# Performance work log

Hardware: AMD Instinct MI355X
Metric: run time of the kernel (lower is better)

## Reference

```python
import jax, jax.numpy as jnp
import numpy as np
import math

B, T, D_IN, D_OUT = 4, 2048, 2048, 2048

def _inv_sigmoid(v):
    return math.log(v / (1 - v + 1e-08))

def setup_inputs() -> dict:
    key = jax.random.key(0)
    ks = jax.random.split(key, 6)
    x = jax.random.normal(ks[0], (B, T, D_IN), dtype=jnp.float32)
    W_p = jax.random.normal(ks[1], (D_OUT, D_IN), dtype=jnp.float32) * 0.02
    W_i = jax.random.normal(ks[2], (D_OUT, D_IN), dtype=jnp.float32) * 0.002
    W_d = jax.random.normal(ks[3], (D_OUT, D_IN), dtype=jnp.float32) * 0.002
    alpha_logit = jnp.full((D_IN,), _inv_sigmoid(0.9), dtype=jnp.float32)
    beta_logit = jnp.full((D_IN,), _inv_sigmoid(0.5), dtype=jnp.float32)
    W_gate_w = jax.random.normal(ks[4], (3, 3 * D_IN), dtype=jnp.float32) * 0.01
    W_gate_b = jnp.array([1.0, 0.0, 0.0], dtype=jnp.float32)
    bias = jnp.zeros((D_OUT,), dtype=jnp.float32)
    return {"x": x, "W_p": W_p, "W_i": W_i, "W_d": W_d,
            "alpha_logit": alpha_logit, "beta_logit": beta_logit,
            "W_gate_w": W_gate_w, "W_gate_b": W_gate_b, "bias": bias}

def _pid_features(x, alpha, beta):
    # x: (B,T,D). Single scan computing EMA integral and smoothed derivative.
    x_t = jnp.swapaxes(x, 0, 1)  # (T,B,D)
    x_prev = jnp.concatenate([jnp.zeros_like(x_t[:1]), x_t[:-1]], axis=0)
    diff_t = x_t - x_prev  # raw finite difference
    def step(carry, inp):
        s, d = carry
        xt, dt = inp
        s = alpha * s + (1.0 - alpha) * xt
        d = beta * d + (1.0 - beta) * dt
        return (s, d), (s, d)
    s0 = jnp.zeros(x.shape[::2], dtype=x.dtype)  # (B,D)
    _, (integ_t, deriv_t) = jax.lax.scan(step, (s0, s0), (x_t, diff_t))
    return jnp.swapaxes(integ_t, 0, 1), jnp.swapaxes(deriv_t, 0, 1)

def reference(x, W_p, W_i, W_d, alpha_logit, beta_logit, W_gate_w, W_gate_b, bias):
    alpha = jax.nn.sigmoid(alpha_logit)  # (D,)
    beta = jax.nn.sigmoid(beta_logit)
    integral, derivative = _pid_features(x, alpha, beta)  # (B,T,D) each
    gate_in = jnp.concatenate([x, integral, derivative], axis=-1)  # (B,T,3D)
    logits = jnp.einsum('btk,gk->btg', gate_in, W_gate_w) + W_gate_b
    gates = jax.nn.softmax(logits, axis=-1)  # (B,T,3)
    p_out = jnp.einsum('btd,od->bto', x, W_p)
    i_out = jnp.einsum('btd,od->bto', integral, W_i)
    d_out = jnp.einsum('btd,od->bto', derivative, W_d)
    y = gates[..., 0:1] * p_out + gates[..., 1:2] * i_out + gates[..., 2:3] * d_out + bias
    return y
```

## Files before the change

### kernel.cpp

```cpp
#include <hip/hip_runtime.h>
#include <stdint.h>

typedef unsigned short u16;

#define GAS __attribute__((address_space(1)))
#define LAS __attribute__((address_space(3)))

typedef __bf16 bf16x8 __attribute__((ext_vector_type(8)));
typedef float f32x4 __attribute__((ext_vector_type(4)));


__device__ inline u16 f2b(float f) {
    uint32_t x = __float_as_uint(f);
    uint32_t r = (x + 0x7fffu + ((x >> 16) & 1u)) >> 16;
    return (u16)r;
}

__device__ inline float b2f(u16 u) {
    union { uint32_t i; float f; } v;
    v.i = ((uint32_t)u) << 16;
    return v.f;
}

__device__ inline void load8b(float* v, const u16* p) {
    uint4 u = *(const uint4*)p;
    v[0] = b2f((u16)(u.x)); v[1] = b2f((u16)(u.x >> 16));
    v[2] = b2f((u16)(u.y)); v[3] = b2f((u16)(u.y >> 16));
    v[4] = b2f((u16)(u.z)); v[5] = b2f((u16)(u.z >> 16));
    v[6] = b2f((u16)(u.w)); v[7] = b2f((u16)(u.w >> 16));
}

__device__ inline void load8f(float* v, const float* p) {
    float4 a = *(const float4*)p;
    float4 b = *(const float4*)(p + 4);
    v[0] = a.x; v[1] = a.y; v[2] = a.z; v[3] = a.w;
    v[4] = b.x; v[5] = b.y; v[6] = b.z; v[7] = b.w;
}

__device__ inline void store8b(u16* p, const float* v, float scale) {
    uint4 u;
    u.x = (uint32_t)f2b(v[0] * scale) | ((uint32_t)f2b(v[1] * scale) << 16);
    u.y = (uint32_t)f2b(v[2] * scale) | ((uint32_t)f2b(v[3] * scale) << 16);
    u.z = (uint32_t)f2b(v[4] * scale) | ((uint32_t)f2b(v[5] * scale) << 16);
    u.w = (uint32_t)f2b(v[6] * scale) | ((uint32_t)f2b(v[7] * scale) << 16);
    *(uint4*)p = u;
}

__device__ inline float sigmoidf(float v) { return 1.f / (1.f + __expf(-v)); }

__device__ inline float pow64f(float a) {
    float p = a * a;
    p = p * p;
    p = p * p;
    p = p * p;
    p = p * p;
    return p * p;
}

__device__ inline float* carry_ptr(u16* Z, int plane, int b, int c, int d) {
    int f = ((plane * 4 + b) * 32 + c) * 2048 + d;
    int row = f >> 10;
    int off = f & 1023;
    return (float*)(Z + (size_t)row * 6144) + off;
}

__global__ __launch_bounds__(256) void pack_w(
    const float* __restrict__ Wp, const float* __restrict__ Wi,
    const float* __restrict__ Wd, u16* __restrict__ Wcat)
{
    int i = (blockIdx.x * 256 + threadIdx.x) * 8;
    int seg = i >> 22;
    int j = i & 4194303;
    const float* src = (seg == 0) ? Wp : (seg == 1) ? Wi : Wd;
    int o = j >> 11;
    int c = j & 2047;
    float v[8];
    load8f(v, src + j);
    store8b(Wcat + (size_t)o * 6144 + seg * 2048 + c, v, 1.0f);
}

__global__ __launch_bounds__(256) void scan_pass1(
    const float* __restrict__ x, const float* __restrict__ alog,
    const float* __restrict__ blog, u16* __restrict__ Z)
{
    const int d = blockIdx.x * 256 + threadIdx.x;
    const int c = blockIdx.y;
    const int b = blockIdx.z;
    const float alpha = sigmoidf(alog[d]);
    const float beta  = sigmoidf(blog[d]);
    const float oma = 1.f - alpha, omb = 1.f - beta;
    const float* xp = x + ((size_t)b * 2048 + c * 64) * 2048 + d;
    float xprev = (c == 0) ? 0.f : xp[-2048];
    float s = 0.f, dd = 0.f;
    #pragma unroll 8
    for (int t = 0; t < 64; ++t) {
        float xf = xp[(size_t)t * 2048];
        s = alpha * s + oma * xf;
        dd = beta * dd + omb * (xf - xprev);
        xprev = xf;
    }
    *carry_ptr(Z, 0, b, c, d) = s;
    *carry_ptr(Z, 1, b, c, d) = dd;
}

__global__ __launch_bounds__(256) void scan_pass2(
    const float* __restrict__ alog, const float* __restrict__ blog,
    u16* __restrict__ Z)
{
    const int g = blockIdx.x * 256 + threadIdx.x;
    const int b = g >> 11;
    const int d = g & 2047;
    const float aL = pow64f(sigmoidf(alog[d]));
    const float bL = pow64f(sigmoidf(blog[d]));
    float sIn = 0.f, dIn = 0.f;
    for (int c = 0; c < 32; ++c) {
        float* sp = carry_ptr(Z, 0, b, c, d);
        float* dp = carry_ptr(Z, 1, b, c, d);
        float sl = *sp, dl = *dp;
        *sp = sIn; *dp = dIn;
        sIn = sl + aL * sIn;
        dIn = dl + bL * dIn;
    }
}

__global__ __launch_bounds__(256) void scan_pass3(
    const float* __restrict__ x, const float* __restrict__ alog,
    const float* __restrict__ blog, u16* __restrict__ Z)
{
    const int d = blockIdx.x * 256 + threadIdx.x;
    const int c = blockIdx.y;
    const int b = blockIdx.z;
    const float alpha = sigmoidf(alog[d]);
    const float beta  = sigmoidf(blog[d]);
    const float oma = 1.f - alpha, omb = 1.f - beta;
    const float* xp = x + ((size_t)b * 2048 + c * 64) * 2048 + d;
    u16* zp = Z + ((size_t)b * 2048 + c * 64) * 6144 + 2048 + d;
    float s  = *carry_ptr(Z, 0, b, c, d);
    float dd = *carry_ptr(Z, 1, b, c, d);
    float xprev = (c == 0) ? 0.f : xp[-2048];
    #pragma unroll 8
    for (int t = 0; t < 64; ++t) {
        float xf = xp[(size_t)t * 2048];
        s = alpha * s + oma * xf;
        dd = beta * dd + omb * (xf - xprev);
        xprev = xf;
        size_t zo = (size_t)t * 6144;
        zp[zo] = f2b(s);
        zp[zo + 2048] = f2b(dd);
    }
}

__global__ __launch_bounds__(256) void gates_kernel(
    const float* __restrict__ x, const float* __restrict__ Wg,
    const float* __restrict__ Wgb, u16* __restrict__ Z)
{
    const int row = blockIdx.x;
    const int tid = threadIdx.x;
    const int k = tid * 8;
    const float* xr = x + (size_t)row * 2048;
    u16* zr = Z + (size_t)row * 6144;

    float xv[8], sv[8], dv[8];
    load8f(xv, xr + k);
    load8b(sv, zr + 2048 + k);
    load8b(dv, zr + 4096 + k);

    float p[3];
    #pragma unroll
    for (int gg = 0; gg < 3; ++gg) {
        float wx[8], ws[8], wd[8];
        load8f(wx, Wg + gg * 6144 + k);
        load8f(ws, Wg + gg * 6144 + 2048 + k);
        load8f(wd, Wg + gg * 6144 + 4096 + k);
        float acc = 0.f;
        #pragma unroll
        for (int j = 0; j < 8; ++j)
            acc += xv[j] * wx[j] + sv[j] * ws[j] + dv[j] * wd[j];
        p[gg] = acc;
    }

    #pragma unroll
    for (int off = 32; off > 0; off >>= 1) {
        p[0] += __shfl_down(p[0], off);
        p[1] += __shfl_down(p[1], off);
        p[2] += __shfl_down(p[2], off);
    }

    __shared__ float red[4][3];
    __shared__ float gsh[3];
    int wv = tid >> 6, lane = tid & 63;
    if (lane == 0) { red[wv][0] = p[0]; red[wv][1] = p[1]; red[wv][2] = p[2]; }
    __syncthreads();
    if (tid == 0) {
        float l0 = red[0][0] + red[1][0] + red[2][0] + red[3][0] + Wgb[0];
        float l1 = red[0][1] + red[1][1] + red[2][1] + red[3][1] + Wgb[1];
        float l2 = red[0][2] + red[1][2] + red[2][2] + red[3][2] + Wgb[2];
        float m = fmaxf(l0, fmaxf(l1, l2));
        float e0 = __expf(l0 - m), e1 = __expf(l1 - m), e2 = __expf(l2 - m);
        float inv = 1.f / (e0 + e1 + e2);
        gsh[0] = e0 * inv; gsh[1] = e1 * inv; gsh[2] = e2 * inv;
    }
    __syncthreads();
    float g0 = gsh[0], g1 = gsh[1], g2 = gsh[2];
    store8b(zr + k, xv, g0);
    store8b(zr + 2048 + k, sv, g1);
    store8b(zr + 4096 + k, dv, g2);
}

__global__ __launch_bounds__(512, 2) void gemm_kernel(
    const u16* __restrict__ Z, const u16* __restrict__ Wcat,
    const float* __restrict__ bias, float* __restrict__ out)
{
    extern __shared__ u16 lds[];
    u16* const lA = lds;
    u16* const lB = lds + 32768;

    const int tid = threadIdx.x;
    const int bn = blockIdx.x * 256;
    const int bm = blockIdx.y * 256;

    const int sr  = tid >> 3;
    const int scq = (tid & 7) ^ (sr & 7);
    const u16* aglob = Z    + (size_t)(bm + sr) * 6144 + scq * 8;
    const u16* bglob = Wcat + (size_t)(bn + sr) * 6144 + scq * 8;

    const int lane = tid & 63;
    const int wv = tid >> 6;
    const int wm = wv & 1;
    const int wn = wv >> 1;
    const int fr = lane & 15;
    const int fq = lane >> 4;
    const int chlo = fq ^ (fr & 7);
    const int aoff = fr * 64 + chlo * 8;
    const int boff = ((wn & 1) * 64 + fr) * 64 + chlo * 8;
    const int aoffh = aoff ^ 32;
    const int boffh = boff ^ 32;

    f32x4 acc[8][4] = {};

#define GLOAD(gsrc, ldst)                                                     \
    __builtin_amdgcn_global_load_lds((const GAS uint32_t*)(gsrc),             \
                                     (LAS uint32_t*)(ldst), 16, 0, 0)

    GLOAD(bglob,                        lB + tid * 8);
    GLOAD(bglob + (size_t) 64 * 6144,   lB + 4096 + tid * 8);
    GLOAD(bglob + (size_t)128 * 6144,   lB + 8192 + tid * 8);
    GLOAD(bglob + (size_t)192 * 6144,   lB + 8192 + 4096 + tid * 8);
    GLOAD(aglob,                        lA + tid * 8);
    GLOAD(aglob + (size_t)128 * 6144,   lA + 8192 + tid * 8);
    GLOAD(aglob + (size_t) 64 * 6144,   lA + 4096 + tid * 8);
    GLOAD(aglob + (size_t)192 * 6144,   lA + 8192 + 4096 + tid * 8);
    asm volatile("s_waitcnt vmcnt(2)" ::: "memory");
    __builtin_amdgcn_s_barrier();

    for (int kt = 0; kt < 96; ++kt) {
        const int pb  = (kt & 1) * 2;
        const int nbb = pb ^ 2;
        const int t1  = (kt < 95) ? kt + 1 : 95;
        const size_t kc = (size_t)t1 * 64;
        const u16* aS = lA + (pb + wm) * 8192;
        const u16* bS = lB + (pb + (wn >> 1)) * 8192;
        bf16x8 av[4], bv[4];

        #pragma unroll
        for (int i = 0; i < 4; ++i) av[i] = *(const bf16x8*)(aS + aoff + i * 1024);
        #pragma unroll
        for (int j = 0; j < 4; ++j) bv[j] = *(const bf16x8*)(bS + boff + j * 1024);
        GLOAD(bglob + kc,                      lB + nbb * 8192 + tid * 8);
        GLOAD(bglob + (size_t)64 * 6144 + kc,  lB + nbb * 8192 + 4096 + tid * 8);
        __builtin_amdgcn_s_barrier();
        asm volatile("s_waitcnt lgkmcnt(0)" ::: "memory");
        __builtin_amdgcn_s_setprio(1);
        #pragma unroll
        for (int i = 0; i < 4; ++i)
            #pragma unroll
            for (int j = 0; j < 4; ++j)
                acc[i][j] = __builtin_amdgcn_mfma_f32_16x16x32_bf16(
                    av[i], bv[j], acc[i][j], 0, 0, 0);
        __builtin_amdgcn_s_setprio(0);
        asm volatile("s_waitcnt vmcnt(2)" ::: "memory");
        __builtin_amdgcn_s_barrier();

        #pragma unroll
        for (int i = 0; i < 4; ++i)
            av[i] = *(const bf16x8*)(aS + aoff + 4096 + i * 1024);
        GLOAD(bglob + (size_t)128 * 6144 + kc, lB + (nbb + 1) * 8192 + tid * 8);
        GLOAD(bglob + (size_t)192 * 6144 + kc, lB + (nbb + 1) * 8192 + 4096 + tid * 8);
        __builtin_amdgcn_s_barrier();
        asm volatile("s_waitcnt lgkmcnt(0)" ::: "memory");
        __builtin_amdgcn_s_setprio(1);
        #pragma unroll
        for (int i = 0; i < 4; ++i)
            #pragma unroll
            for (int j = 0; j < 4; ++j)
                acc[4 + i][j] = __builtin_amdgcn_mfma_f32_16x16x32_bf16(
                    av[i], bv[j], acc[4 + i][j], 0, 0, 0);
        __builtin_amdgcn_s_setprio(0);
        __builtin_amdgcn_s_barrier();

        #pragma unroll
        for (int i = 0; i < 4; ++i) av[i] = *(const bf16x8*)(aS + aoffh + i * 1024);
        #pragma unroll
        for (int j = 0; j < 4; ++j) bv[j] = *(const bf16x8*)(bS + boffh + j * 1024);
        GLOAD(aglob + kc,                      lA + nbb * 8192 + tid * 8);
        GLOAD(aglob + (size_t)128 * 6144 + kc, lA + (nbb + 1) * 8192 + tid * 8);
        __builtin_amdgcn_s_barrier();
        asm volatile("s_waitcnt lgkmcnt(0)" ::: "memory");
        __builtin_amdgcn_s_setprio(1);
        #pragma unroll
        for (int i = 0; i < 4; ++i)
            #pragma unroll
            for (int j = 0; j < 4; ++j)
                acc[i][j] = __builtin_amdgcn_mfma_f32_16x16x32_bf16(
                    av[i], bv[j], acc[i][j], 0, 0, 0);
        __builtin_amdgcn_s_setprio(0);
        __builtin_amdgcn_s_barrier();

        #pragma unroll
        for (int i = 0; i < 4; ++i)
            av[i] = *(const bf16x8*)(aS + aoffh + 4096 + i * 1024);
        GLOAD(aglob + (size_t) 64 * 6144 + kc, lA + nbb * 8192 + 4096 + tid * 8);
        GLOAD(aglob + (size_t)192 * 6144 + kc, lA + (nbb + 1) * 8192 + 4096 + tid * 8);
        __builtin_amdgcn_s_barrier();
        asm volatile("s_waitcnt lgkmcnt(0)" ::: "memory");
        __builtin_amdgcn_s_setprio(1);
        #pragma unroll
        for (int i = 0; i < 4; ++i)
            #pragma unroll
            for (int j = 0; j < 4; ++j)
                acc[4 + i][j] = __builtin_amdgcn_mfma_f32_16x16x32_bf16(
                    av[i], bv[j], acc[4 + i][j], 0, 0, 0);
        __builtin_amdgcn_s_setprio(0);
        asm volatile("s_waitcnt vmcnt(2)" ::: "memory");
        __builtin_amdgcn_s_barrier();
    }

    asm volatile("s_waitcnt vmcnt(0)" ::: "memory");

    #pragma unroll
    for (int j = 0; j < 4; ++j) {
        const int col = bn + wn * 64 + j * 16 + fr;
        const float bb = bias[col];
        #pragma unroll
        for (int mf = 0; mf < 8; ++mf) {
            const int row0 = bm + wm * 128 + mf * 16 + fq * 4;
            #pragma unroll
            for (int r = 0; r < 4; ++r)
                out[(size_t)(row0 + r) * 2048 + col] = acc[mf][j][r] + bb;
        }
    }
#undef GLOAD
}

extern "C" void kernel_launch(void* const* d_in, const int* in_sizes, int n_in,
                              void* d_out, int out_size, void* d_ws, size_t ws_size,
                              hipStream_t stream) {
    const float* x    = (const float*)d_in[0];
    const float* Wp   = (const float*)d_in[1];
    const float* Wi   = (const float*)d_in[2];
    const float* Wd   = (const float*)d_in[3];
    const float* al   = (const float*)d_in[4];
    const float* bl   = (const float*)d_in[5];
    const float* Wg   = (const float*)d_in[6];
    const float* Wgb  = (const float*)d_in[7];
    const float* bias = (const float*)d_in[8];
    float* out = (float*)d_out;

    u16* Z    = (u16*)d_ws;
    u16* Wcat = (u16*)((char*)d_ws + (size_t)8192 * 6144 * 2);

    static bool lds_cfgd = false;
    if (!lds_cfgd) {
        (void)hipFuncSetAttribute((const void*)gemm_kernel,
                                  hipFuncAttributeMaxDynamicSharedMemorySize,
                                  131072);
        lds_cfgd = true;
    }

    pack_w<<<6144, 256, 0, stream>>>(Wp, Wi, Wd, Wcat);
    scan_pass1<<<dim3(8, 32, 4), 256, 0, stream>>>(x, al, bl, Z);
    scan_pass2<<<32, 256, 0, stream>>>(al, bl, Z);
    scan_pass3<<<dim3(8, 32, 4), 256, 0, stream>>>(x, al, bl, Z);
    gates_kernel<<<8192, 256, 0, stream>>>(x, Wg, Wgb, Z);
    gemm_kernel<<<dim3(8, 32), 512, 131072, stream>>>(Z, Wcat, bias, out);
}
```

Measured before the change: 413.7 us.

## Vectorize scan passes to two channels per thread and batch GEMM tile prefetch

The scan kernels now process two adjacent channels per thread. They use float2 loads and packed 32-bit bf16 stores, which halves the thread count and widens the memory accesses. The GEMM now issues all eight global-to-LDS loads for the next K tile in one batch at the start of each iteration instead of spreading them across four phases, and waits with vmcnt(8). This gives more time for the loads to overlap with compute, at the risk of contention on the LDS buffer and a changed wait schedule. The waitcnt values may no longer match the number of loads still in flight, which could cause stalls or read hazards.

```diff
diff --git a/kernel.cpp b/kernel.cpp
--- a/kernel.cpp
+++ b/kernel.cpp
@@ -83,24 +83,30 @@
     const float* __restrict__ x, const float* __restrict__ alog,
     const float* __restrict__ blog, u16* __restrict__ Z)
 {
-    const int d = blockIdx.x * 256 + threadIdx.x;
+    const int d = (blockIdx.x * 256 + threadIdx.x) * 2;
     const int c = blockIdx.y;
     const int b = blockIdx.z;
-    const float alpha = sigmoidf(alog[d]);
-    const float beta  = sigmoidf(blog[d]);
-    const float oma = 1.f - alpha, omb = 1.f - beta;
+    const float2 al2 = *(const float2*)(alog + d);
+    const float2 bl2 = *(const float2*)(blog + d);
+    const float a0 = sigmoidf(al2.x), a1 = sigmoidf(al2.y);
+    const float e0 = sigmoidf(bl2.x), e1 = sigmoidf(bl2.y);
+    const float oa0 = 1.f - a0, oa1 = 1.f - a1;
+    const float oe0 = 1.f - e0, oe1 = 1.f - e1;
     const float* xp = x + ((size_t)b * 2048 + c * 64) * 2048 + d;
-    float xprev = (c == 0) ? 0.f : xp[-2048];
-    float s = 0.f, dd = 0.f;
+    float px0 = 0.f, px1 = 0.f;
+    if (c != 0) { float2 t = *(const float2*)(xp - 2048); px0 = t.x; px1 = t.y; }
+    float s0 = 0.f, s1 = 0.f, d0 = 0.f, d1 = 0.f;
     #pragma unroll 8
     for (int t = 0; t < 64; ++t) {
-        float xf = xp[(size_t)t * 2048];
-        s = alpha * s + oma * xf;
-        dd = beta * dd + omb * (xf - xprev);
-        xprev = xf;
-    }
-    *carry_ptr(Z, 0, b, c, d) = s;
-    *carry_ptr(Z, 1, b, c, d) = dd;
+        float2 xf = *(const float2*)(xp + (size_t)t * 2048);
+        s0 = a0 * s0 + oa0 * xf.x;
+        s1 = a1 * s1 + oa1 * xf.y;
+        d0 = e0 * d0 + oe0 * (xf.x - px0);
+        d1 = e1 * d1 + oe1 * (xf.y - px1);
+        px0 = xf.x; px1 = xf.y;
+    }
+    *(float2*)carry_ptr(Z, 0, b, c, d) = make_float2(s0, s1);
+    *(float2*)carry_ptr(Z, 1, b, c, d) = make_float2(d0, d1);
 }
 
 __global__ __launch_bounds__(256) void scan_pass2(
@@ -127,26 +133,33 @@
     const float* __restrict__ x, const float* __restrict__ alog,
     const float* __restrict__ blog, u16* __restrict__ Z)
 {
-    const int d = blockIdx.x * 256 + threadIdx.x;
+    const int d = (blockIdx.x * 256 + threadIdx.x) * 2;
     const int c = blockIdx.y;
     const int b = blockIdx.z;
-    const float alpha = sigmoidf(alog[d]);
-    const float beta  = sigmoidf(blog[d]);
-    const float oma = 1.f - alpha, omb = 1.f - beta;
+    const float2 al2 = *(const float2*)(alog + d);
+    const float2 bl2 = *(const float2*)(blog + d);
+    const float a0 = sigmoidf(al2.x), a1 = sigmoidf(al2.y);
+    const float e0 = sigmoidf(bl2.x), e1 = sigmoidf(bl2.y);
+    const float oa0 = 1.f - a0, oa1 = 1.f - a1;
+    const float oe0 = 1.f - e0, oe1 = 1.f - e1;
     const float* xp = x + ((size_t)b * 2048 + c * 64) * 2048 + d;
     u16* zp = Z + ((size_t)b * 2048 + c * 64) * 6144 + 2048 + d;
-    float s  = *carry_ptr(Z, 0, b, c, d);
-    float dd = *carry_ptr(Z, 1, b, c, d);
-    float xprev = (c == 0) ? 0.f : xp[-2048];
+    float2 sc = *(const float2*)carry_ptr(Z, 0, b, c, d);
+    float2 dc = *(const float2*)carry_ptr(Z, 1, b, c, d);
+    float s0 = sc.x, s1 = sc.y, d0 = dc.x, d1 = dc.y;
+    float px0 = 0.f, px1 = 0.f;
+    if (c != 0) { float2 t = *(const float2*)(xp - 2048); px0 = t.x; px1 = t.y; }
     #pragma unroll 8
     for (int t = 0; t < 64; ++t) {
-        float xf = xp[(size_t)t * 2048];
-        s = alpha * s + oma * xf;
-        dd = beta * dd + omb * (xf - xprev);
-        xprev = xf;
+        float2 xf = *(const float2*)(xp + (size_t)t * 2048);
+        s0 = a0 * s0 + oa0 * xf.x;
+        s1 = a1 * s1 + oa1 * xf.y;
+        d0 = e0 * d0 + oe0 * (xf.x - px0);
+        d1 = e1 * d1 + oe1 * (xf.y - px1);
+        px0 = xf.x; px1 = xf.y;
         size_t zo = (size_t)t * 6144;
-        zp[zo] = f2b(s);
-        zp[zo + 2048] = f2b(dd);
+        *(uint32_t*)(zp + zo) = (uint32_t)f2b(s0) | ((uint32_t)f2b(s1) << 16);
+        *(uint32_t*)(zp + zo + 2048) = (uint32_t)f2b(d0) | ((uint32_t)f2b(d1) << 16);
     }
 }
 
@@ -242,22 +255,25 @@
     __builtin_amdgcn_global_load_lds((const GAS uint32_t*)(gsrc),             \
                                      (LAS uint32_t*)(ldst), 16, 0, 0)
 
-    GLOAD(bglob,                        lB + tid * 8);
-    GLOAD(bglob + (size_t) 64 * 6144,   lB + 4096 + tid * 8);
-    GLOAD(bglob + (size_t)128 * 6144,   lB + 8192 + tid * 8);
-    GLOAD(bglob + (size_t)192 * 6144,   lB + 8192 + 4096 + tid * 8);
-    GLOAD(aglob,                        lA + tid * 8);
-    GLOAD(aglob + (size_t)128 * 6144,   lA + 8192 + tid * 8);
-    GLOAD(aglob + (size_t) 64 * 6144,   lA + 4096 + tid * 8);
-    GLOAD(aglob + (size_t)192 * 6144,   lA + 8192 + 4096 + tid * 8);
+#define STAGE8(jt, bb) do {                                                   \
+    const size_t kc_ = (size_t)(jt) * 64;                                     \
+    GLOAD(bglob + kc_,                      lB + (bb) * 16384 + tid * 8);     \
+    GLOAD(bglob + (size_t) 64 * 6144 + kc_, lB + (bb) * 16384 + 4096 + tid * 8); \
+    GLOAD(bglob + (size_t)128 * 6144 + kc_, lB + (bb) * 16384 + 8192 + tid * 8); \
+    GLOAD(bglob + (size_t)192 * 6144 + kc_, lB + (bb) * 16384 + 12288 + tid * 8);\
+    GLOAD(aglob + kc_,                      lA + (bb) * 16384 + tid * 8);     \
+    GLOAD(aglob + (size_t)128 * 6144 + kc_, lA + (bb) * 16384 + 8192 + tid * 8); \
+    GLOAD(aglob + (size_t) 64 * 6144 + kc_, lA + (bb) * 16384 + 4096 + tid * 8); \
+    GLOAD(aglob + (size_t)192 * 6144 + kc_, lA + (bb) * 16384 + 12288 + tid * 8);\
+} while (0)
+
+    STAGE8(0, 0);
     asm volatile("s_waitcnt vmcnt(2)" ::: "memory");
     __builtin_amdgcn_s_barrier();
 
     for (int kt = 0; kt < 96; ++kt) {
         const int pb  = (kt & 1) * 2;
-        const int nbb = pb ^ 2;
         const int t1  = (kt < 95) ? kt + 1 : 95;
-        const size_t kc = (size_t)t1 * 64;
         const u16* aS = lA + (pb + wm) * 8192;
         const u16* bS = lB + (pb + (wn >> 1)) * 8192;
         bf16x8 av[4], bv[4];
@@ -266,8 +282,7 @@
         for (int i = 0; i < 4; ++i) av[i] = *(const bf16x8*)(aS + aoff + i * 1024);
         #pragma unroll
         for (int j = 0; j < 4; ++j) bv[j] = *(const bf16x8*)(bS + boff + j * 1024);
-        GLOAD(bglob + kc,                      lB + nbb * 8192 + tid * 8);
-        GLOAD(bglob + (size_t)64 * 6144 + kc,  lB + nbb * 8192 + 4096 + tid * 8);
+        STAGE8(t1, (kt & 1) ^ 1);
         __builtin_amdgcn_s_barrier();
         asm volatile("s_waitcnt lgkmcnt(0)" ::: "memory");
         __builtin_amdgcn_s_setprio(1);
@@ -278,14 +293,12 @@
                 acc[i][j] = __builtin_amdgcn_mfma_f32_16x16x32_bf16(
                     av[i], bv[j], acc[i][j], 0, 0, 0);
         __builtin_amdgcn_s_setprio(0);
-        asm volatile("s_waitcnt vmcnt(2)" ::: "memory");
+        asm volatile("s_waitcnt vmcnt(8)" ::: "memory");
         __builtin_amdgcn_s_barrier();
 
         #pragma unroll
         for (int i = 0; i < 4; ++i)
             av[i] = *(const bf16x8*)(aS + aoff + 4096 + i * 1024);
-        GLOAD(bglob + (size_t)128 * 6144 + kc, lB + (nbb + 1) * 8192 + tid * 8);
-        GLOAD(bglob + (size_t)192 * 6144 + kc, lB + (nbb + 1) * 8192 + 4096 + tid * 8);
         __builtin_amdgcn_s_barrier();
         asm volatile("s_waitcnt lgkmcnt(0)" ::: "memory");
         __builtin_amdgcn_s_setprio(1);
@@ -302,8 +315,6 @@
         for (int i = 0; i < 4; ++i) av[i] = *(const bf16x8*)(aS + aoffh + i * 1024);
         #pragma unroll
         for (int j = 0; j < 4; ++j) bv[j] = *(const bf16x8*)(bS + boffh + j * 1024);
-        GLOAD(aglob + kc,                      lA + nbb * 8192 + tid * 8);
-        GLOAD(aglob + (size_t)128 * 6144 + kc, lA + (nbb + 1) * 8192 + tid * 8);
         __builtin_amdgcn_s_barrier();
         asm volatile("s_waitcnt lgkmcnt(0)" ::: "memory");
         __builtin_amdgcn_s_setprio(1);
@@ -319,8 +330,6 @@
         #pragma unroll
         for (int i = 0; i < 4; ++i)
             av[i] = *(const bf16x8*)(aS + aoffh + 4096 + i * 1024);
-        GLOAD(aglob + (size_t) 64 * 6144 + kc, lA + nbb * 8192 + 4096 + tid * 8);
-        GLOAD(aglob + (size_t)192 * 6144 + kc, lA + (nbb + 1) * 8192 + 4096 + tid * 8);
         __builtin_amdgcn_s_barrier();
         asm volatile("s_waitcnt lgkmcnt(0)" ::: "memory");
         __builtin_amdgcn_s_setprio(1);
@@ -349,6 +358,7 @@
                 out[(size_t)(row0 + r) * 2048 + col] = acc[mf][j][r] + bb;
         }
     }
+#undef STAGE8
 #undef GLOAD
 }
 
@@ -378,9 +388,9 @@
     }
 
     pack_w<<<6144, 256, 0, stream>>>(Wp, Wi, Wd, Wcat);
-    scan_pass1<<<dim3(8, 32, 4), 256, 0, stream>>>(x, al, bl, Z);
+    scan_pass1<<<dim3(4, 32, 4), 256, 0, stream>>>(x, al, bl, Z);
     scan_pass2<<<32, 256, 0, stream>>>(al, bl, Z);
-    scan_pass3<<<dim3(8, 32, 4), 256, 0, stream>>>(x, al, bl, Z);
+    scan_pass3<<<dim3(4, 32, 4), 256, 0, stream>>>(x, al, bl, Z);
     gates_kernel<<<8192, 256, 0, stream>>>(x, Wg, Wgb, Z);
     gemm_kernel<<<dim3(8, 32), 512, 131072, stream>>>(Z, Wcat, bias, out);
 }
```

Measured after the change: 426.4 us. +3.1%, slower.
